# Performance work log

Measured on AMD Instinct MI355X. Metric: run time of the kernel, lower is better.

## Reference

```python
import jax, jax.numpy as jnp
import numpy as np

B = 65536
IN = 64
OUT = 256
D = 4
P = D * (D + 1) // 2  # total (w1, W2) pairs across all terms


def setup_inputs() -> dict:
    key = jax.random.key(0)
    ks = jax.random.split(key, 6)
    s = 1.0 / np.sqrt(IN)
    return {
        "x": jax.random.normal(ks[0], (B, IN), dtype=jnp.float32),
        "d0": jax.random.uniform(ks[1], (1, OUT), dtype=jnp.float32, minval=-s, maxval=s),
        "d1t_w": jax.random.uniform(ks[2], (OUT, IN), dtype=jnp.float32, minval=-s, maxval=s),
        "d1_w": jax.random.uniform(ks[3], (D, OUT, IN), dtype=jnp.float32, minval=-s, maxval=s),
        "dn_w1": jax.random.uniform(ks[4], (P, IN), dtype=jnp.float32, minval=-s, maxval=s),
        "dn_w2": jax.random.uniform(ks[5], (P, OUT, IN), dtype=jnp.float32, minval=-s, maxval=s),
    }


def reference(x, d0, d1t_w, d1_w, dn_w1, dn_w2):
    # res = d0 + d1t(x) + sum_i (x @ d1_i.T) * prod_{j<=i} (x @ (W2_ij * w1_ij).T)
    # The factorization (x @ (W2 * w1).T) is exactly equal to the original
    # Linear(in,1)(tmp_dt * (tx * W2)) chain, without the [B,out,in] intermediate.
    res = d0 + x @ d1t_w.T  # [B, OUT]
    p = 0
    for i in range(D):
        tmp = x @ d1_w[i].T  # [B, OUT]
        for _ in range(i + 1):
            M = dn_w2[p] * dn_w1[p][None, :]  # [OUT, IN]
            tmp = tmp * (x @ M.T)             # [B, OUT]
            p += 1
        res = res + tmp
    return res
```

## Files before the change

kernel.cpp:

```cpp
#include <hip/hip_runtime.h>
#include <hip/hip_bf16.h>

#define BATCH 65536
#define INF   64
#define OUTF  256
#define NMAT  15
#define RPB   256
#define LDSW  68

typedef __bf16 bf16x8 __attribute__((ext_vector_type(8)));
typedef float  f32x4  __attribute__((ext_vector_type(4)));

__device__ __forceinline__ unsigned short f2bf(float f) {
    unsigned int u = __float_as_uint(f);
    unsigned int r = (u + 0x7FFFu + ((u >> 16) & 1u)) >> 16;
    return (unsigned short)r;
}

__device__ __forceinline__ void wload(bf16x8& d, const void* p) {
    asm volatile("global_load_dwordx4 %0, %1, off" : "=v"(d) : "v"(p));
}

__global__ void prep(const float* __restrict__ x,
                     const float* __restrict__ d1t_w,
                     const float* __restrict__ d1_w,
                     const float* __restrict__ dn_w1,
                     const float* __restrict__ dn_w2,
                     unsigned short* __restrict__ wcs,
                     unsigned short* __restrict__ xs) {
    const int idx = blockIdx.x * 256 + threadIdx.x;

    {
        const int row = idx >> 3, cc = idx & 7;
        const int s = cc >> 2, g = cc & 3;
        const int grp = row >> 4, r = row & 15;
        const float* xp = x + (size_t)row * INF + cc * 8;
        f32x4 v0 = *(const f32x4*)xp;
        f32x4 v1 = *(const f32x4*)(xp + 4);
        bf16x8 fr;
#pragma unroll
        for (int j = 0; j < 4; ++j) { fr[j] = (__bf16)v0[j]; fr[4 + j] = (__bf16)v1[j]; }
        *(bf16x8*)((char*)xs + (size_t)grp * 2048 + s * 1024 + g * 256 + r * 16) = fr;
    }

    if (idx < NMAT * OUTF * INF / 8) {
        const signed char kind[NMAT] = {0,1,2,1,2,2,1,2,2,2,1,2,2,2,2};
        const signed char sidx[NMAT] = {0,0,0,1,1,2,2,3,4,5,3,6,7,8,9};
        const int slot = idx >> 11, rem8 = idx & 2047;
        const int o = rem8 >> 3, cc = rem8 & 7;
        const int s = cc >> 2, g = cc & 3;
        const int i0 = cc * 8;
        const int cs = o >> 4, l = o & 15;
        const int k = kind[slot], si = sidx[slot];
        unsigned short o8[8];
#pragma unroll
        for (int j = 0; j < 8; ++j) {
            const int e = o * INF + i0 + j;
            float v;
            if (k == 0)      v = d1t_w[e];
            else if (k == 1) v = d1_w[si * OUTF * INF + e];
            else             v = dn_w2[si * OUTF * INF + e] * dn_w1[si * INF + i0 + j];
            o8[j] = f2bf(v);
        }
        char* dst = (char*)wcs + (((size_t)slot * 16 + cs) * 2 + s) * 1024 + g * 256 + l * 16;
        *(bf16x8*)dst = *(bf16x8*)o8;
    }
}

__global__ __launch_bounds__(512, 4) void taylor_kernel(
    const unsigned short* __restrict__ xs, const float* __restrict__ d0w,
    const unsigned short* __restrict__ wcs, float* __restrict__ out)
{
    __shared__ float sbuf[2][2][32 * LDSW];

    const int lane  = threadIdx.x & 63;
    const int wv    = threadIdx.x >> 6;
    const int strip = wv >> 1;
    const int role  = wv & 1;
    const int l15   = lane & 15;
    const int g     = lane >> 4;
    const int cg    = blockIdx.x >> 8;
    const int rc    = blockIdx.x & 255;
    const int cs    = cg * 4 + strip;

    const int MA[8] = {0, 1, 2, 6, 7, 8, 9, 9};
    const int MB[8] = {3, 4, 5, 10, 11, 12, 13, 14};
    bf16x8 b[8][2];
    const char* wb0 = (const char*)wcs + lane * 16;
#pragma unroll
    for (int i = 0; i < 8; ++i) {
        const int m = role ? MB[i] : MA[i];
        if (role == 0 && i == 7) continue;
        const char* wp = wb0 + (((size_t)m * 16 + cs) * 2) * 1024;
        wload(b[i][0], wp);
        wload(b[i][1], wp + 1024);
    }
    asm volatile("s_waitcnt vmcnt(0)" ::: "memory");
    __builtin_amdgcn_sched_barrier(0);

    const f32x4 d0v = *(const f32x4*)(d0w + cs * 16 + g * 4);

    const size_t row0 = (size_t)rc * RPB;
    const char* xbase = (const char*)xs + (row0 >> 4) * 2048 + lane * 16;

    bf16x8 u00 = *(const bf16x8*)(xbase);
    bf16x8 u01 = *(const bf16x8*)(xbase + 1024);
    bf16x8 u10 = *(const bf16x8*)(xbase + 2048);
    bf16x8 u11 = *(const bf16x8*)(xbase + 3072);

#pragma unroll
    for (int t = 0; t < 8; ++t) {
        f32x4 res0, res1, tmp0, tmp1, y0, y1;
        const f32x4 z = {0.f, 0.f, 0.f, 0.f};
        __builtin_amdgcn_s_setprio(1);
#define Y4(bi, c0)                                                                  \
        y0 = __builtin_amdgcn_mfma_f32_16x16x32_bf16(b[bi][0], u00, c0, 0, 0, 0);   \
        y1 = __builtin_amdgcn_mfma_f32_16x16x32_bf16(b[bi][0], u10, c0, 0, 0, 0);   \
        y0 = __builtin_amdgcn_mfma_f32_16x16x32_bf16(b[bi][1], u01, y0, 0, 0, 0);   \
        y1 = __builtin_amdgcn_mfma_f32_16x16x32_bf16(b[bi][1], u11, y1, 0, 0, 0);
        if (role == 0) {
            Y4(0, d0v) res0 = y0; res1 = y1;
            Y4(1, z)   tmp0 = y0; tmp1 = y1;
            Y4(2, z)   tmp0 *= y0; tmp1 *= y1; res0 += tmp0; res1 += tmp1;
            Y4(3, z)   tmp0 = y0; tmp1 = y1;
            Y4(4, z)   tmp0 *= y0; tmp1 *= y1;
            Y4(5, z)   tmp0 *= y0; tmp1 *= y1;
            Y4(6, z)   tmp0 *= y0; tmp1 *= y1; res0 += tmp0; res1 += tmp1;
        } else {
            Y4(0, z)   tmp0 = y0; tmp1 = y1;
            Y4(1, z)   tmp0 *= y0; tmp1 *= y1;
            Y4(2, z)   tmp0 *= y0; tmp1 *= y1; res0 = tmp0; res1 = tmp1;
            Y4(3, z)   tmp0 = y0; tmp1 = y1;
            Y4(4, z)   tmp0 *= y0; tmp1 *= y1;
            Y4(5, z)   tmp0 *= y0; tmp1 *= y1;
            Y4(6, z)   tmp0 *= y0; tmp1 *= y1;
            Y4(7, z)   tmp0 *= y0; tmp1 *= y1; res0 += tmp0; res1 += tmp1;
        }
#undef Y4
        __builtin_amdgcn_s_setprio(0);

        if (t < 7) {
            const char* p = xbase + (size_t)(t + 1) * 4096;
            u00 = *(const bf16x8*)(p);
            u01 = *(const bf16x8*)(p + 1024);
            u10 = *(const bf16x8*)(p + 2048);
            u11 = *(const bf16x8*)(p + 3072);
        }

        float* sb = &sbuf[t & 1][role][0];
        const int colw = strip * 16 + g * 4;
        *(f32x4*)&sb[l15 * LDSW + colw]        = res0;
        *(f32x4*)&sb[(16 + l15) * LDSW + colw] = res1;
        asm volatile("s_waitcnt lgkmcnt(0)\n\ts_barrier" ::: "memory");

        const float* pA = &sbuf[t & 1][0][0];
        const float* pB = &sbuf[t & 1][1][0];
        const int rr = threadIdx.x >> 4;
        const int c4 = (threadIdx.x & 15) * 4;
        f32x4 v = *(const f32x4*)&pA[rr * LDSW + c4];
        v = v + *(const f32x4*)&pB[rr * LDSW + c4];
        float* op = out + (row0 + (size_t)t * 32 + rr) * OUTF + cg * 64 + c4;
        __builtin_nontemporal_store(v, (f32x4*)op);
    }
}

extern "C" void kernel_launch(void* const* d_in, const int* in_sizes, int n_in,
                              void* d_out, int out_size, void* d_ws, size_t ws_size,
                              hipStream_t stream) {
    const float* x    = (const float*)d_in[0];
    const float* d0   = (const float*)d_in[1];
    const float* d1t  = (const float*)d_in[2];
    const float* d1w  = (const float*)d_in[3];
    const float* dnw1 = (const float*)d_in[4];
    const float* dnw2 = (const float*)d_in[5];
    unsigned short* wcs = (unsigned short*)d_ws;
    float* out = (float*)d_out;

    unsigned short* xsb = (unsigned short*)((char*)d_ws + 512 * 1024);
    prep<<<BATCH * INF / 8 / 256, 256, 0, stream>>>(x, d1t, d1w, dnw1, dnw2, wcs, xsb);
    taylor_kernel<<<4 * (BATCH / RPB), 512, 0, stream>>>(xsb, d0, wcs, out);
}
```

Baseline: 41.25 us.

## Halve block width to 256 threads and interleave independent MFMA chains

Each block now covers 32 output columns with 4 waves instead of 64 columns with 8 waves. The grid doubles to 8 column groups, and the LDS stride and the final reduce/store indexing shrink to match. The MFMA sequence is restructured so two independent projection chains are in flight at once, which exposes more instruction-level parallelism around the elementwise products. The cost is that each x tile is now loaded by twice as many blocks, and launch bounds allow fewer resident blocks per CU.

```diff
diff --git a/kernel.cpp b/kernel.cpp
--- a/kernel.cpp
+++ b/kernel.cpp
@@ -6,7 +6,7 @@
 #define OUTF  256
 #define NMAT  15
 #define RPB   256
-#define LDSW  68
+#define LDSW  36
 
 typedef __bf16 bf16x8 __attribute__((ext_vector_type(8)));
 typedef float  f32x4  __attribute__((ext_vector_type(4)));
@@ -67,7 +67,7 @@
     }
 }
 
-__global__ __launch_bounds__(512, 4) void taylor_kernel(
+__global__ __launch_bounds__(256, 3) void taylor_kernel(
     const unsigned short* __restrict__ xs, const float* __restrict__ d0w,
     const unsigned short* __restrict__ wcs, float* __restrict__ out)
 {
@@ -81,7 +81,7 @@
     const int g     = lane >> 4;
     const int cg    = blockIdx.x >> 8;
     const int rc    = blockIdx.x & 255;
-    const int cs    = cg * 4 + strip;
+    const int cs    = cg * 2 + strip;
 
     const int MA[8] = {0, 1, 2, 6, 7, 8, 9, 9};
     const int MB[8] = {3, 4, 5, 10, 11, 12, 13, 14};
@@ -99,7 +99,6 @@
     __builtin_amdgcn_sched_barrier(0);
 
     const f32x4 d0v = *(const f32x4*)(d0w + cs * 16 + g * 4);
-
     const size_t row0 = (size_t)rc * RPB;
     const char* xbase = (const char*)xs + (row0 >> 4) * 2048 + lane * 16;
 
@@ -110,33 +109,50 @@
 
 #pragma unroll
     for (int t = 0; t < 8; ++t) {
-        f32x4 res0, res1, tmp0, tmp1, y0, y1;
+        f32x4 res0, res1, tmp0, tmp1;
+        f32x4 y0a, y0b, y1a, y1b;
         const f32x4 z = {0.f, 0.f, 0.f, 0.f};
         __builtin_amdgcn_s_setprio(1);
-#define Y4(bi, c0)                                                                  \
-        y0 = __builtin_amdgcn_mfma_f32_16x16x32_bf16(b[bi][0], u00, c0, 0, 0, 0);   \
-        y1 = __builtin_amdgcn_mfma_f32_16x16x32_bf16(b[bi][0], u10, c0, 0, 0, 0);   \
-        y0 = __builtin_amdgcn_mfma_f32_16x16x32_bf16(b[bi][1], u01, y0, 0, 0, 0);   \
-        y1 = __builtin_amdgcn_mfma_f32_16x16x32_bf16(b[bi][1], u11, y1, 0, 0, 0);
+#define YM(bi, ya, yb, c0)                                                          \
+        ya = __builtin_amdgcn_mfma_f32_16x16x32_bf16(b[bi][0], u00, c0, 0, 0, 0);   \
+        yb = __builtin_amdgcn_mfma_f32_16x16x32_bf16(b[bi][0], u10, c0, 0, 0, 0);   \
+        ya = __builtin_amdgcn_mfma_f32_16x16x32_bf16(b[bi][1], u01, ya, 0, 0, 0);   \
+        yb = __builtin_amdgcn_mfma_f32_16x16x32_bf16(b[bi][1], u11, yb, 0, 0, 0);
+
         if (role == 0) {
-            Y4(0, d0v) res0 = y0; res1 = y1;
-            Y4(1, z)   tmp0 = y0; tmp1 = y1;
-            Y4(2, z)   tmp0 *= y0; tmp1 *= y1; res0 += tmp0; res1 += tmp1;
-            Y4(3, z)   tmp0 = y0; tmp1 = y1;
-            Y4(4, z)   tmp0 *= y0; tmp1 *= y1;
-            Y4(5, z)   tmp0 *= y0; tmp1 *= y1;
-            Y4(6, z)   tmp0 *= y0; tmp1 *= y1; res0 += tmp0; res1 += tmp1;
+            YM(0, y0a, y0b, d0v)
+            YM(1, y1a, y1b, z)
+            res0 = y0a;  res1 = y0b;
+            tmp0 = y1a;  tmp1 = y1b;
+            YM(2, y0a, y0b, z)
+            YM(3, y1a, y1b, z)
+            tmp0 *= y0a; tmp1 *= y0b; res0 += tmp0; res1 += tmp1;
+            tmp0 = y1a;  tmp1 = y1b;
+            YM(4, y0a, y0b, z)
+            YM(5, y1a, y1b, z)
+            tmp0 *= y0a; tmp1 *= y0b;
+            tmp0 *= y1a; tmp1 *= y1b;
+            YM(6, y0a, y0b, z)
+            tmp0 *= y0a; tmp1 *= y0b; res0 += tmp0; res1 += tmp1;
         } else {
-            Y4(0, z)   tmp0 = y0; tmp1 = y1;
-            Y4(1, z)   tmp0 *= y0; tmp1 *= y1;
-            Y4(2, z)   tmp0 *= y0; tmp1 *= y1; res0 = tmp0; res1 = tmp1;
-            Y4(3, z)   tmp0 = y0; tmp1 = y1;
-            Y4(4, z)   tmp0 *= y0; tmp1 *= y1;
-            Y4(5, z)   tmp0 *= y0; tmp1 *= y1;
-            Y4(6, z)   tmp0 *= y0; tmp1 *= y1;
-            Y4(7, z)   tmp0 *= y0; tmp1 *= y1; res0 += tmp0; res1 += tmp1;
+            YM(0, y0a, y0b, z)
+            YM(1, y1a, y1b, z)
+            tmp0 = y0a * y1a;  tmp1 = y0b * y1b;
+            YM(2, y0a, y0b, z)
+            YM(3, y1a, y1b, z)
+            res0 = tmp0 * y0a; res1 = tmp1 * y0b;
+            tmp0 = y1a;        tmp1 = y1b;
+            YM(4, y0a, y0b, z)
+            YM(5, y1a, y1b, z)
+            tmp0 *= y0a; tmp1 *= y0b;
+            tmp0 *= y1a; tmp1 *= y1b;
+            YM(6, y0a, y0b, z)
+            YM(7, y1a, y1b, z)
+            tmp0 *= y0a; tmp1 *= y0b;
+            tmp0 *= y1a; tmp1 *= y1b;
+            res0 += tmp0; res1 += tmp1;
         }
-#undef Y4
+#undef YM
         __builtin_amdgcn_s_setprio(0);
 
         if (t < 7) {
@@ -155,11 +171,11 @@
 
         const float* pA = &sbuf[t & 1][0][0];
         const float* pB = &sbuf[t & 1][1][0];
-        const int rr = threadIdx.x >> 4;
-        const int c4 = (threadIdx.x & 15) * 4;
+        const int rr = threadIdx.x >> 3;
+        const int c4 = (threadIdx.x & 7) * 4;
         f32x4 v = *(const f32x4*)&pA[rr * LDSW + c4];
         v = v + *(const f32x4*)&pB[rr * LDSW + c4];
-        float* op = out + (row0 + (size_t)t * 32 + rr) * OUTF + cg * 64 + c4;
+        float* op = out + (row0 + (size_t)t * 32 + rr) * OUTF + cg * 32 + c4;
         __builtin_nontemporal_store(v, (f32x4*)op);
     }
 }
@@ -178,5 +194,5 @@
 
     unsigned short* xsb = (unsigned short*)((char*)d_ws + 512 * 1024);
     prep<<<BATCH * INF / 8 / 256, 256, 0, stream>>>(x, d1t, d1w, dnw1, dnw2, wcs, xsb);
-    taylor_kernel<<<4 * (BATCH / RPB), 512, 0, stream>>>(xsb, d0, wcs, out);
+    taylor_kernel<<<8 * (BATCH / RPB), 256, 0, stream>>>(xsb, d0, wcs, out);
 }
```

After: 42.78 us. 1.04x slower.
